# Kernel tuning notes

Hardware: AMD Instinct MI355X
Metric: run time of the kernel (lower is better)

## Reference

```python
import jax, jax.numpy as jnp
import numpy as np

B = 4
NB = 8192   # points per batch
MB = 2048   # query points per batch
C_IN = 64
RADII = (0.2, 0.4)
NSAMPLES = (16, 32)
EPS = 1e-5


def setup_inputs() -> dict:
    key = jax.random.key(0)
    ks = jax.random.split(key, 8)
    inp = {}
    inp["xyz"] = jax.random.uniform(ks[0], (B * NB, 3), jnp.float32)
    inp["features"] = jax.random.normal(ks[1], (B * NB, C_IN), jnp.float32)
    inp["new_xyz"] = jax.random.uniform(ks[2], (B * MB, 3), jnp.float32)
    inp["xyz_batch_cnt"] = jnp.full((B,), NB, jnp.int32)
    inp["new_xyz_batch_cnt"] = jnp.full((B,), MB, jnp.int32)
    cin = C_IN + 3  # use_xyz=True concatenates relative xyz
    for s in range(2):
        k0, k1 = jax.random.split(ks[3 + s])
        inp[f"w{s}0"] = jax.random.normal(k0, (128, cin), jnp.float32) * (2.0 / cin) ** 0.5
        inp[f"g{s}0"] = jnp.ones((128,), jnp.float32)
        inp[f"b{s}0"] = jnp.zeros((128,), jnp.float32)
        inp[f"w{s}1"] = jax.random.normal(k1, (128, 128), jnp.float32) * (2.0 / 128) ** 0.5
        inp[f"g{s}1"] = jnp.ones((128,), jnp.float32)
        inp[f"b{s}1"] = jnp.zeros((128,), jnp.float32)
    return inp


def _ball_query(new_b, xyz_b, radius, nsample):
    # new_b: (B, M, 3), xyz_b: (B, N, 3)
    n = xyz_b.shape[1]
    # squared distances via the quadratic expansion (avoids (B,M,N,3) temp)
    d2 = (jnp.sum(new_b * new_b, -1)[:, :, None]
          + jnp.sum(xyz_b * xyz_b, -1)[:, None, :]
          - 2.0 * jnp.einsum('bmc,bnc->bmn', new_b, xyz_b))
    in_ball = d2 < radius * radius
    # first-nsample-in-original-order semantics of the CUDA ball query
    order_key = jnp.where(in_ball, jnp.arange(n, dtype=jnp.int32)[None, None, :], n)
    idxs = jnp.sort(order_key, axis=-1)[..., :nsample]        # (B, M, nsample)
    valid = idxs < n
    first = idxs[..., :1]                                     # pad with first found idx
    idx = jnp.where(valid, idxs, first)
    empty = ~valid[..., 0]                                    # no neighbor in ball
    idx = jnp.where(empty[..., None], 0, idx)
    return idx, empty


def _bn_relu(x, g, b):
    # training-mode BatchNorm2d over (M, nsample) per channel, then ReLU
    mean = jnp.mean(x, axis=(0, 1))
    var = jnp.var(x, axis=(0, 1))
    return jax.nn.relu((x - mean) * jax.lax.rsqrt(var + EPS) * g + b)


def _scale(xyz_b, feat_b, new_b, radius, nsample, w0, g0, b0, w1, g1, b1):
    idx, empty = _ball_query(new_b, xyz_b, radius, nsample)
    gather = jax.vmap(lambda pts, i: pts[i])                  # per-batch gather
    gx = gather(xyz_b, idx) - new_b[:, :, None, :]            # (B, M, ns, 3)
    gf = gather(feat_b, idx)                                  # (B, M, ns, C)
    g = jnp.concatenate([gx, gf], axis=-1)                    # use_xyz=True
    g = jnp.where(empty[..., None, None], 0.0, g)             # zero empty balls
    g = g.reshape(-1, nsample, g.shape[-1])                   # (M_total, ns, 3+C)
    h = _bn_relu(jnp.einsum('mnc,oc->mno', g, w0), g0, b0)    # shared 1x1 conv
    h = _bn_relu(jnp.einsum('mnc,oc->mno', h, w1), g1, b1)
    return jnp.max(h, axis=1)                                 # max_pool over ns


def reference(xyz, features, new_xyz, xyz_batch_cnt, new_xyz_batch_cnt,
              w00, g00, b00, w01, g01, b01,
              w10, g10, b10, w11, g11, b11):
    b = xyz_batch_cnt.shape[0]
    xyz_b = xyz.reshape(b, -1, 3)
    feat_b = features.reshape(b, -1, features.shape[-1])
    new_b = new_xyz.reshape(b, -1, 3)
    f0 = _scale(xyz_b, feat_b, new_b, RADII[0], NSAMPLES[0], w00, g00, b00, w01, g01, b01)
    f1 = _scale(xyz_b, feat_b, new_b, RADII[1], NSAMPLES[1], w10, g10, b10, w11, g11, b11)
    return new_xyz, jnp.concatenate([f0, f1], axis=1)         # (M_total, 256)
```

## Files before the change

### kernel.cpp

```cpp
#include <hip/hip_runtime.h>
#include <stdio.h>

#define NBP   8192
#define MTOT  8192
#define CIN   64
#define CO    128

#define EPR(...) do { fprintf(stderr, __VA_ARGS__); fflush(stderr); } while (0)

typedef short short8 __attribute__((ext_vector_type(8)));
typedef float floatx4 __attribute__((ext_vector_type(4)));
typedef unsigned short ushort;
typedef ushort ushort4v __attribute__((ext_vector_type(4)));

__device__ __forceinline__ ushort f2b(float f)
{
    union { unsigned int i; float f; } x; x.f = f;
    return (ushort)((x.i + 0x7fffu + ((x.i >> 16) & 1u)) >> 16);
}
__device__ __forceinline__ float b2f(ushort u)
{
    union { unsigned int i; float f; } x; x.i = ((unsigned int)u) << 16;
    return x.f;
}
__device__ __forceinline__ void split_rne(float v, ushort& h, ushort& l)
{
    ushort hh = f2b(v);
    h = hh; l = f2b(v - b2f(hh));
}

__global__ void __launch_bounds__(256, 1) StackSAModuleMSG_85761906966880_kernel(
    const float* __restrict__ xyz, const float* __restrict__ nxyz,
    float* __restrict__ out, float* __restrict__ stats,
    const float* __restrict__ feat, ushort* __restrict__ fh,
    int* __restrict__ idx0, int* __restrict__ idx1,
    int* __restrict__ empty0, int* __restrict__ empty1,
    const float* __restrict__ w00, const float* __restrict__ w01,
    const float* __restrict__ w10, const float* __restrict__ w11,
    ushort* __restrict__ wh00, ushort* __restrict__ wl00,
    ushort* __restrict__ wh01, ushort* __restrict__ wl01,
    ushort* __restrict__ wh10, ushort* __restrict__ wl10,
    ushort* __restrict__ wh11, ushort* __restrict__ wl11)
{
    if (blockIdx.x < MTOT/4) {
        const double r2a = 0.2 * 0.2;
        const double r2b = 0.4 * 0.4;
        int m    = blockIdx.x * 4 + (threadIdx.x >> 6);
        int lane = threadIdx.x & 63;
        int b    = m >> 11;
        int base = b * NBP;

        double nx = (double)nxyz[3*m+0];
        double ny = (double)nxyz[3*m+1];
        double nz = (double)nxyz[3*m+2];
        double nn = nx*nx + ny*ny + nz*nz;

        int cnt0 = 0, cnt1 = 0;
        int first0 = base, first1 = base;
        unsigned long long lt = (1ull << lane) - 1ull;

        for (int j = 0; j < NBP; j += 64) {
            int gi = base + j + lane;
            double px = (double)xyz[3*gi+0];
            double py = (double)xyz[3*gi+1];
            double pz = (double)xyz[3*gi+2];
            double pp = px*px + py*py + pz*pz;
            double dt = nx*px + ny*py + nz*pz;
            double d2 = nn + pp - 2.0*dt;
            bool in0 = d2 < r2a;
            bool in1 = d2 < r2b;
            unsigned long long m0 = __ballot(in0);
            unsigned long long m1 = __ballot(in1);
            if (in0) {
                int p0 = cnt0 + __popcll(m0 & lt);
                if (p0 < 16) idx0[m*16 + p0] = gi;
            }
            if (in1) {
                int p1 = cnt1 + __popcll(m1 & lt);
                if (p1 < 32) idx1[m*32 + p1] = gi;
            }
            if (cnt0 == 0 && m0) first0 = base + j + (__ffsll((long long)m0) - 1);
            if (cnt1 == 0 && m1) first1 = base + j + (__ffsll((long long)m1) - 1);
            cnt0 += __popcll(m0);
            cnt1 += __popcll(m1);
            if (cnt0 >= 16 && cnt1 >= 32) break;
        }
        int c0 = cnt0 < 16 ? cnt0 : 16;
        int c1 = cnt1 < 32 ? cnt1 : 32;
        if (lane >= c0 && lane < 16) idx0[m*16 + lane] = first0;
        if (lane >= c1 && lane < 32) idx1[m*32 + lane] = first1;
        if (lane == 0) { empty0[m] = (cnt0 == 0); empty1[m] = (cnt1 == 0); }
    } else {
        int i = (blockIdx.x - MTOT/4) * 256 + threadIdx.x;
        if (i < 1024) stats[i] = 0.f;
        if (i < MTOT*3) out[i] = nxyz[i];
        if (i < 128*128) {
            split_rne(w01[i], wh01[i], wl01[i]);
            split_rne(w11[i], wh11[i], wl11[i]);
        }
        if (i < 128*96) {
            int o = i / 96, kd = i - o*96;
            int c = (kd < 64) ? (kd + 3) : ((kd < 67) ? (kd - 64) : -1);
            float a = (c >= 0) ? w00[o*67 + c] : 0.f;
            split_rne(a, wh00[i], wl00[i]);
            float b = (c >= 0) ? w10[o*67 + c] : 0.f;
            split_rne(b, wh10[i], wl10[i]);
        }
        {
            float4 v = *(const float4*)(feat + (size_t)4*i);
            ushort4v h;
            h[0] = f2b(v.x); h[1] = f2b(v.y); h[2] = f2b(v.z); h[3] = f2b(v.w);
            *(ushort4v*)(fh + (size_t)4*i) = h;
        }
    }
}

template<int NS, int GM>
__device__ __forceinline__ void gather128(
    const ushort* __restrict__ fh,
    const float* __restrict__ xyz, const float* __restrict__ nxyz,
    const int* __restrict__ idx, unsigned em, int m0, int t, ushort* ah)
{
    constexpr int ROWS = NS*GM;
    const long long ib = (long long)m0 * NS;
    const short8 Z8 = {0,0,0,0,0,0,0,0};
#pragma unroll
    for (int e = t; e < ROWS*8; e += 256) {
        int n = e >> 3, c8 = e & 7;
        int gi = idx[ib + n];
        short8 v = *(const short8*)(fh + (size_t)gi*CIN + 8*c8);
        if ((em >> (n / NS)) & 1u) v = Z8;
        *(short8*)(ah + n*136 + 8*c8) = v;
    }
#pragma unroll
    for (int e = t; e < ROWS*4; e += 256) {
        int n = e >> 2, k3 = e & 3;
        short8 v = Z8;
        if (k3 == 0) {
            int g = n / NS;
            if (!((em >> g) & 1u)) {
                int gi = idx[ib + n];
#pragma unroll
                for (int c = 0; c < 3; c++)
                    v[c] = (short)f2b(xyz[3*gi+c] - nxyz[3*(m0+g)+c]);
            }
        }
        *(short8*)(ah + n*136 + 64 + 8*k3) = v;
    }
}

template<int NS, int GM>
__device__ __forceinline__ void stats1_body(
    const ushort* __restrict__ fh,
    const float* __restrict__ xyz, const float* __restrict__ nxyz,
    const int* __restrict__ idx, const int* __restrict__ empty,
    const ushort* __restrict__ wh0, float* __restrict__ part,
    int bx, int t, ushort* ah)
{
    int m0 = bx * GM;
    int wv = t >> 6, lane = t & 63, l16 = lane & 15, qo = lane >> 4;
    int n0 = 32*wv;

    short8 bh[3][2];
#pragma unroll
    for (int ks = 0; ks < 3; ks++)
#pragma unroll
        for (int nt = 0; nt < 2; nt++)
            bh[ks][nt] = *(const short8*)(wh0 +
                (long long)(n0 + 16*nt + l16)*96 + ks*32 + qo*8);

    unsigned em = 0;
#pragma unroll
    for (int g = 0; g < GM; g++) em |= (empty[m0 + g] ? 1u : 0u) << g;
    gather128<NS, GM>(fh, xyz, nxyz, idx, em, m0, t, ah);
    __syncthreads();

    floatx4 acc[8][2];
#pragma unroll
    for (int i = 0; i < 8; i++) {
        acc[i][0] = (floatx4){0.f,0.f,0.f,0.f};
        acc[i][1] = (floatx4){0.f,0.f,0.f,0.f};
    }
#pragma unroll
    for (int ks = 0; ks < 3; ks++) {
        int kb = ks*32 + qo*8;
#pragma unroll
        for (int mt = 0; mt < 8; mt++) {
            int ao = (16*mt + l16)*136 + kb;
            short8 fh8 = *(const short8*)(ah + ao);
#pragma unroll
            for (int nt = 0; nt < 2; nt++)
                acc[mt][nt] = __builtin_amdgcn_mfma_f32_16x16x32_bf16(
                                  fh8, bh[ks][nt], acc[mt][nt], 0, 0, 0);
        }
    }

    float sum[2] = {0.f,0.f}, sq[2] = {0.f,0.f};
#pragma unroll
    for (int mt = 0; mt < 8; mt++)
#pragma unroll
        for (int nt = 0; nt < 2; nt++)
#pragma unroll
            for (int r = 0; r < 4; r++) {
                float a = acc[mt][nt][r];
                sum[nt] += a; sq[nt] = fmaf(a, a, sq[nt]);
            }
#pragma unroll
    for (int nt = 0; nt < 2; nt++) {
        sum[nt] += __shfl_xor(sum[nt], 16); sum[nt] += __shfl_xor(sum[nt], 32);
        sq[nt]  += __shfl_xor(sq[nt],  16); sq[nt]  += __shfl_xor(sq[nt],  32);
    }
    if (lane < 16) {
#pragma unroll
        for (int nt = 0; nt < 2; nt++) {
            int c = n0 + 16*nt + lane;
            part[(long long)bx*256 + c]       = sum[nt];
            part[(long long)bx*256 + 128 + c] = sq[nt];
        }
    }
}

__global__ void __launch_bounds__(256, 4) sa_stats1_both(
    const ushort* __restrict__ fh,
    const float* __restrict__ xyz, const float* __restrict__ nxyz,
    const int* __restrict__ idx0, const int* __restrict__ empty0,
    const ushort* __restrict__ wh00, float* __restrict__ partA,
    const int* __restrict__ idx1, const int* __restrict__ empty1,
    const ushort* __restrict__ wh10, float* __restrict__ partB)
{
    __shared__ ushort ah[128*136];
    int t = threadIdx.x;
    if (blockIdx.x < MTOT/8)
        stats1_body<16,8>(fh, xyz, nxyz, idx0, empty0, wh00, partA,
                          blockIdx.x, t, ah);
    else
        stats1_body<32,4>(fh, xyz, nxyz, idx1, empty1, wh10, partB,
                          blockIdx.x - MTOT/8, t, ah);
}

template<int NS, int GM>
__device__ __forceinline__ void fused_body(
    const ushort* __restrict__ fh,
    const float* __restrict__ xyz, const float* __restrict__ nxyz,
    const int* __restrict__ idx, const int* __restrict__ empty,
    const ushort* __restrict__ wh0, const ushort* __restrict__ wl0,
    const ushort* __restrict__ wh1, const ushort* __restrict__ wl1,
    const float* __restrict__ g0, const float* __restrict__ b0,
    const float* __restrict__ s1sum, const float* __restrict__ s1sq,
    float* __restrict__ part, float* __restrict__ mxo, float* __restrict__ mno,
    float invN, int bx, int t,
    ushort* ah, float* kv, float* sv)
{
    const int TPG = NS/16;
    int m0 = bx * GM;
    int wv = t >> 6, lane = t & 63, l16 = lane & 15, qo = lane >> 4;
    int n0 = 32*wv;

    if (t < 128) {
        float mean = s1sum[t] * invN;
        float var  = s1sq[t] * invN - mean * mean;
        float k    = rsqrtf(var + 1e-5f) * g0[t];
        kv[t] = k;
        sv[t] = b0[t] - mean * k;
    }

    const long long wrow0 = (long long)(n0 + l16);
    const long long wrow1 = (long long)(n0 + 16 + l16);

    short8 wsh[2][2], wsl[2][2];
#pragma unroll
    for (int ks = 0; ks < 2; ks++) {
        wsh[ks][0] = *(const short8*)(wh0 + wrow0*96 + ks*32 + qo*8);
        wsl[ks][0] = *(const short8*)(wl0 + wrow0*96 + ks*32 + qo*8);
        wsh[ks][1] = *(const short8*)(wh0 + wrow1*96 + ks*32 + qo*8);
        wsl[ks][1] = *(const short8*)(wl0 + wrow1*96 + ks*32 + qo*8);
    }

    unsigned em = 0;
#pragma unroll
    for (int g = 0; g < GM; g++) em |= (empty[m0 + g] ? 1u : 0u) << g;
    gather128<NS, GM>(fh, xyz, nxyz, idx, em, m0, t, ah);
    __syncthreads();

    floatx4 acc[8][2];
#pragma unroll
    for (int i = 0; i < 8; i++) {
        acc[i][0] = (floatx4){0.f,0.f,0.f,0.f};
        acc[i][1] = (floatx4){0.f,0.f,0.f,0.f};
    }

#pragma unroll
    for (int mt = 0; mt < 8; mt++) {
        short8 fh8 = *(const short8*)(ah + (16*mt + l16)*136 + qo*8);
#pragma unroll
        for (int nt = 0; nt < 2; nt++) {
            acc[mt][nt] = __builtin_amdgcn_mfma_f32_16x16x32_bf16(
                              fh8, wsl[0][nt], acc[mt][nt], 0, 0, 0);
            acc[mt][nt] = __builtin_amdgcn_mfma_f32_16x16x32_bf16(
                              fh8, wsh[0][nt], acc[mt][nt], 0, 0, 0);
        }
    }
    wsh[0][0] = *(const short8*)(wh0 + wrow0*96 + 64 + qo*8);
    wsl[0][0] = *(const short8*)(wl0 + wrow0*96 + 64 + qo*8);
    wsh[0][1] = *(const short8*)(wh0 + wrow1*96 + 64 + qo*8);
    wsl[0][1] = *(const short8*)(wl0 + wrow1*96 + 64 + qo*8);
#pragma unroll
    for (int mt = 0; mt < 8; mt++) {
        short8 fh8 = *(const short8*)(ah + (16*mt + l16)*136 + 32 + qo*8);
#pragma unroll
        for (int nt = 0; nt < 2; nt++) {
            acc[mt][nt] = __builtin_amdgcn_mfma_f32_16x16x32_bf16(
                              fh8, wsl[1][nt], acc[mt][nt], 0, 0, 0);
            acc[mt][nt] = __builtin_amdgcn_mfma_f32_16x16x32_bf16(
                              fh8, wsh[1][nt], acc[mt][nt], 0, 0, 0);
        }
    }
#pragma unroll
    for (int mt = 0; mt < 8; mt++) {
        short8 fh8 = *(const short8*)(ah + (16*mt + l16)*136 + 64 + qo*8);
#pragma unroll
        for (int nt = 0; nt < 2; nt++) {
            acc[mt][nt] = __builtin_amdgcn_mfma_f32_16x16x32_bf16(
                              fh8, wsl[0][nt], acc[mt][nt], 0, 0, 0);
            acc[mt][nt] = __builtin_amdgcn_mfma_f32_16x16x32_bf16(
                              fh8, wsh[0][nt], acc[mt][nt], 0, 0, 0);
        }
    }

    __syncthreads();

#pragma unroll
    for (int nt = 0; nt < 2; nt++) {
        int c = n0 + 16*nt + l16;
        float k = kv[c], s = sv[c];
#pragma unroll
        for (int mt = 0; mt < 8; mt++) {
            int rbase = 16*mt + qo*4;
#pragma unroll
            for (int r = 0; r < 4; r += 2) {
                float h0 = fmaxf(fmaf(acc[mt][nt][r],   k, s), 0.f);
                float h1 = fmaxf(fmaf(acc[mt][nt][r+1], k, s), 0.f);
                unsigned int pk;
                asm("v_cvt_pk_bf16_f32 %0, %1, %2"
                    : "=v"(pk) : "v"(h0), "v"(h1));
                ah[(rbase + r    )*136 + c] = (ushort)(pk & 0xffffu);
                ah[(rbase + r + 1)*136 + c] = (ushort)(pk >> 16);
            }
        }
    }

#pragma unroll
    for (int ks = 0; ks < 2; ks++) {
        wsh[ks][0] = *(const short8*)(wh1 + wrow0*128 + ks*32 + qo*8);
        wsl[ks][0] = *(const short8*)(wl1 + wrow0*128 + ks*32 + qo*8);
        wsh[ks][1] = *(const short8*)(wh1 + wrow1*128 + ks*32 + qo*8);
        wsl[ks][1] = *(const short8*)(wl1 + wrow1*128 + ks*32 + qo*8);
    }
    __syncthreads();

#pragma unroll
    for (int i = 0; i < 8; i++) {
        acc[i][0] = (floatx4){0.f,0.f,0.f,0.f};
        acc[i][1] = (floatx4){0.f,0.f,0.f,0.f};
    }
#pragma unroll
    for (int mt = 0; mt < 8; mt++) {
        short8 fh8 = *(const short8*)(ah + (16*mt + l16)*136 + qo*8);
#pragma unroll
        for (int nt = 0; nt < 2; nt++) {
            acc[mt][nt] = __builtin_amdgcn_mfma_f32_16x16x32_bf16(
                              fh8, wsl[0][nt], acc[mt][nt], 0, 0, 0);
            acc[mt][nt] = __builtin_amdgcn_mfma_f32_16x16x32_bf16(
                              fh8, wsh[0][nt], acc[mt][nt], 0, 0, 0);
        }
    }
    wsh[0][0] = *(const short8*)(wh1 + wrow0*128 + 64 + qo*8);
    wsl[0][0] = *(const short8*)(wl1 + wrow0*128 + 64 + qo*8);
    wsh[0][1] = *(const short8*)(wh1 + wrow1*128 + 64 + qo*8);
    wsl[0][1] = *(const short8*)(wl1 + wrow1*128 + 64 + qo*8);
#pragma unroll
    for (int mt = 0; mt < 8; mt++) {
        short8 fh8 = *(const short8*)(ah + (16*mt + l16)*136 + 32 + qo*8);
#pragma unroll
        for (int nt = 0; nt < 2; nt++) {
            acc[mt][nt] = __builtin_amdgcn_mfma_f32_16x16x32_bf16(
                              fh8, wsl[1][nt], acc[mt][nt], 0, 0, 0);
            acc[mt][nt] = __builtin_amdgcn_mfma_f32_16x16x32_bf16(
                              fh8, wsh[1][nt], acc[mt][nt], 0, 0, 0);
        }
    }
    wsh[1][0] = *(const short8*)(wh1 + wrow0*128 + 96 + qo*8);
    wsl[1][0] = *(const short8*)(wl1 + wrow0*128 + 96 + qo*8);
    wsh[1][1] = *(const short8*)(wh1 + wrow1*128 + 96 + qo*8);
    wsl[1][1] = *(const short8*)(wl1 + wrow1*128 + 96 + qo*8);
#pragma unroll
    for (int mt = 0; mt < 8; mt++) {
        short8 fh8 = *(const short8*)(ah + (16*mt + l16)*136 + 64 + qo*8);
#pragma unroll
        for (int nt = 0; nt < 2; nt++) {
            acc[mt][nt] = __builtin_amdgcn_mfma_f32_16x16x32_bf16(
                              fh8, wsl[0][nt], acc[mt][nt], 0, 0, 0);
            acc[mt][nt] = __builtin_amdgcn_mfma_f32_16x16x32_bf16(
                              fh8, wsh[0][nt], acc[mt][nt], 0, 0, 0);
        }
    }
#pragma unroll
    for (int mt = 0; mt < 8; mt++) {
        short8 fh8 = *(const short8*)(ah + (16*mt + l16)*136 + 96 + qo*8);
#pragma unroll
        for (int nt = 0; nt < 2; nt++) {
            acc[mt][nt] = __builtin_amdgcn_mfma_f32_16x16x32_bf16(
                              fh8, wsl[1][nt], acc[mt][nt], 0, 0, 0);
            acc[mt][nt] = __builtin_amdgcn_mfma_f32_16x16x32_bf16(
                              fh8, wsh[1][nt], acc[mt][nt], 0, 0, 0);
        }
    }

    float sum[2] = {0.f,0.f}, sq[2] = {0.f,0.f};
    float Mx[GM][2], Mn[GM][2];
#pragma unroll
    for (int g = 0; g < GM; g++) {
        Mx[g][0] = -3.4e38f; Mx[g][1] = -3.4e38f;
        Mn[g][0] =  3.4e38f; Mn[g][1] =  3.4e38f;
    }
#pragma unroll
    for (int mt = 0; mt < 8; mt++) {
        int gg = mt / TPG;
#pragma unroll
        for (int nt = 0; nt < 2; nt++)
#pragma unroll
            for (int r = 0; r < 4; r++) {
                float a = acc[mt][nt][r];
                sum[nt] += a; sq[nt] = fmaf(a, a, sq[nt]);
                Mx[gg][nt] = fmaxf(Mx[gg][nt], a);
                Mn[gg][nt] = fminf(Mn[gg][nt], a);
            }
    }
#pragma unroll
    for (int nt = 0; nt < 2; nt++) {
        sum[nt] += __shfl_xor(sum[nt], 16); sum[nt] += __shfl_xor(sum[nt], 32);
        sq[nt]  += __shfl_xor(sq[nt],  16); sq[nt]  += __shfl_xor(sq[nt],  32);
#pragma unroll
        for (int g = 0; g < GM; g++) {
            Mx[g][nt] = fmaxf(Mx[g][nt], __shfl_xor(Mx[g][nt], 16));
            Mx[g][nt] = fmaxf(Mx[g][nt], __shfl_xor(Mx[g][nt], 32));
            Mn[g][nt] = fminf(Mn[g][nt], __shfl_xor(Mn[g][nt], 16));
            Mn[g][nt] = fminf(Mn[g][nt], __shfl_xor(Mn[g][nt], 32));
        }
    }
    if (lane < 16) {
#pragma unroll
        for (int nt = 0; nt < 2; nt++) {
            int c = n0 + 16*nt + lane;
            part[(long long)bx*256 + c]       = sum[nt];
            part[(long long)bx*256 + 128 + c] = sq[nt];
#pragma unroll
            for (int g = 0; g < GM; g++) {
                mxo[(long long)(m0+g)*128 + c] = Mx[g][nt];
                mno[(long long)(m0+g)*128 + c] = Mn[g][nt];
            }
        }
    }
}

__global__ void __launch_bounds__(256, 4) sa_fused_both(
    const ushort* __restrict__ fh,
    const float* __restrict__ xyz, const float* __restrict__ nxyz,
    const int* __restrict__ idx0, const int* __restrict__ empty0,
    const ushort* __restrict__ wh00, const ushort* __restrict__ wl00,
    const ushort* __restrict__ wh01, const ushort* __restrict__ wl01,
    const float* __restrict__ g00, const float* __restrict__ b00,
    const float* __restrict__ s1sumA, const float* __restrict__ s1sqA,
    float* __restrict__ partA, float* __restrict__ mx0, float* __restrict__ mn0,
    float invN0,
    const int* __restrict__ idx1, const int* __restrict__ empty1,
    const ushort* __restrict__ wh10, const ushort* __restrict__ wl10,
    const ushort* __restrict__ wh11, const ushort* __restrict__ wl11,
    const float* __restrict__ g10, const float* __restrict__ b10,
    const float* __restrict__ s1sumB, const float* __restrict__ s1sqB,
    float* __restrict__ partB, float* __restrict__ mx1, float* __restrict__ mn1,
    float invN1)
{
    __shared__ ushort ah[128*136];
    __shared__ float kv[128], sv[128];
    int t = threadIdx.x;
    if (blockIdx.x < MTOT/8)
        fused_body<16,8>(fh, xyz, nxyz, idx0, empty0,
                         wh00, wl00, wh01, wl01, g00, b00, s1sumA, s1sqA,
                         partA, mx0, mn0, invN0, blockIdx.x, t,
                         ah, kv, sv);
    else
        fused_body<32,4>(fh, xyz, nxyz, idx1, empty1,
                         wh10, wl10, wh11, wl11, g10, b10, s1sumB, s1sqB,
                         partB, mx1, mn1, invN1, blockIdx.x - MTOT/8, t,
                         ah, kv, sv);
}

__global__ void __launch_bounds__(256, 1) sa_reduce2(
    const float* __restrict__ partA, int nbA, float* __restrict__ dstA,
    const float* __restrict__ partB, int nbB, float* __restrict__ dstB)
{
    __shared__ float red[256];
    int t = threadIdx.x;
    const float* part; float* dst; int nb, b;
    if (blockIdx.x < 256) { part = partA; dst = dstA; nb = nbA; b = blockIdx.x; }
    else                  { part = partB; dst = dstB; nb = nbB; b = blockIdx.x - 256; }
    float s = 0.f;
    for (int i = t; i < nb; i += 256) s += part[(long long)i*256 + b];
    red[t] = s;
    __syncthreads();
    for (int off = 128; off > 0; off >>= 1) {
        if (t < off) red[t] += red[t + off];
        __syncthreads();
    }
    if (t == 0) dst[b] = red[0];
}

__global__ void __launch_bounds__(256, 1) sa_pass3b(
    const float* __restrict__ mx0, const float* __restrict__ mn0,
    const float* __restrict__ g01, const float* __restrict__ b01,
    const float* __restrict__ mx1, const float* __restrict__ mn1,
    const float* __restrict__ g11, const float* __restrict__ b11,
    const float* __restrict__ stats, float* __restrict__ outp,
    float invN0, float invN1)
{
    int i = blockIdx.x * 256 + threadIdx.x;
    int m = i >> 8, o = i & 255;
    bool sc1 = o >= 128;
    int oc = o & 127;
    const float* sm = sc1 ? (stats + 768) : (stats + 256);
    const float* sp = sc1 ? (stats + 896) : (stats + 384);
    float invN = sc1 ? invN1 : invN0;
    float gg   = sc1 ? g11[oc] : g01[oc];
    float bb   = sc1 ? b11[oc] : b01[oc];
    float mean = sm[oc] * invN;
    float var  = sp[oc] * invN - mean * mean;
    float k    = rsqrtf(var + 1e-5f) * gg;
    float sh   = bb - mean * k;
    long long mi = (long long)m * 128 + oc;
    float v;
    if (k >= 0.f) v = sc1 ? mx1[mi] : mx0[mi];
    else          v = sc1 ? mn1[mi] : mn0[mi];
    float r = fmaf(v, k, sh);
    outp[i] = r > 0.f ? r : 0.f;
}

extern "C" void kernel_launch(void* const* d_in, const int* in_sizes, int n_in,
                              void* d_out, int out_size, void* d_ws, size_t ws_size,
                              hipStream_t stream)
{
    const float* xyz  = (const float*)d_in[0];
    const float* feat = (const float*)d_in[1];
    const float* nxyz = (const float*)d_in[2];
    const float* w00 = (const float*)d_in[5];
    const float* g00 = (const float*)d_in[6];
    const float* b00 = (const float*)d_in[7];
    const float* w01 = (const float*)d_in[8];
    const float* g01 = (const float*)d_in[9];
    const float* b01 = (const float*)d_in[10];
    const float* w10 = (const float*)d_in[11];
    const float* g10 = (const float*)d_in[12];
    const float* b10 = (const float*)d_in[13];
    const float* w11 = (const float*)d_in[14];
    const float* g11 = (const float*)d_in[15];
    const float* b11 = (const float*)d_in[16];
    float* out = (float*)d_out;

    char*  wsb    = (char*)d_ws;
    float* stats  = (float*)(wsb);
    int*   idx0   = (int*)(wsb + 4096);
    int*   idx1   = (int*)(wsb + 4096 + 524288);
    int*   empty0 = (int*)(wsb + 4096 + 524288 + 1048576);
    int*   empty1 = (int*)(wsb + 4096 + 524288 + 1048576 + 32768);
    ushort* fh    = (ushort*)(wsb + 2000000);
    float* mx0    = (float*)(wsb + 150000000);
    float* mn0    = (float*)(wsb + 155000000);
    float* mx1    = (float*)(wsb + 160000000);
    float* mn1    = (float*)(wsb + 165000000);
    ushort* wh01  = (ushort*)(wsb + 170000000);
    ushort* wl01  = (ushort*)(wsb + 171000000);
    ushort* wh11  = (ushort*)(wsb + 172000000);
    ushort* wl11  = (ushort*)(wsb + 173000000);
    ushort* wh00  = (ushort*)(wsb + 174000000);
    ushort* wl00  = (ushort*)(wsb + 175000000);
    ushort* wh10  = (ushort*)(wsb + 176000000);
    ushort* wl10  = (ushort*)(wsb + 177000000);
    float* partA  = (float*)(wsb + 180000000);
    float* partB  = (float*)(wsb + 183000000);

    const float invN0 = 1.0f / (float)(MTOT*16);
    const float invN1 = 1.0f / (float)(MTOT*32);
    float* fout = out + MTOT*3;

    StackSAModuleMSG_85761906966880_kernel<<<MTOT/4 + 2048, 256, 0, stream>>>(
        xyz, nxyz, out, stats, feat, fh,
        idx0, idx1, empty0, empty1,
        w00, w01, w10, w11,
        wh00, wl00, wh01, wl01, wh10, wl10, wh11, wl11);

    sa_stats1_both<<<MTOT/8 + MTOT/4, 256, 0, stream>>>(
        fh, xyz, nxyz,
        idx0, empty0, wh00, partA,
        idx1, empty1, wh10, partB);

    sa_reduce2<<<512, 256, 0, stream>>>(partA, MTOT/8, stats + 0,
                                        partB, MTOT/4, stats + 512);

    sa_fused_both<<<MTOT/8 + MTOT/4, 256, 0, stream>>>(
        fh, xyz, nxyz,
        idx0, empty0, wh00, wl00, wh01, wl01, g00, b00,
        stats + 0, stats + 128, partA, mx0, mn0, invN0,
        idx1, empty1, wh10, wl10, wh11, wl11, g10, b10,
        stats + 512, stats + 640, partB, mx1, mn1, invN1);

    sa_reduce2<<<512, 256, 0, stream>>>(partA, MTOT/8, stats + 256,
                                        partB, MTOT/4, stats + 768);

    sa_pass3b<<<(MTOT*256)/256, 256, 0, stream>>>(
        mx0, mn0, g01, b01, mx1, mn1, g11, b11, stats, fout, invN0, invN1);

    hipError_t e = hipGetLastError();
    if (e != hipSuccess) EPR("[KL] enqueue err=%d (%s)\n", (int)e, hipGetErrorString(e));
}
```

Measured before the change: 208.8 us.

## Replace per-block BN partials and reduce kernels with striped atomic accumulation

Result: faster. 201.0 us (-3.7%).

```diff
diff --git a/kernel.cpp b/kernel.cpp
--- a/kernel.cpp
+++ b/kernel.cpp
@@ -31,7 +31,7 @@
 
 __global__ void __launch_bounds__(256, 1) StackSAModuleMSG_85761906966880_kernel(
     const float* __restrict__ xyz, const float* __restrict__ nxyz,
-    float* __restrict__ out, float* __restrict__ stats,
+    float* __restrict__ out, float* __restrict__ scop,
     const float* __restrict__ feat, ushort* __restrict__ fh,
     int* __restrict__ idx0, int* __restrict__ idx1,
     int* __restrict__ empty0, int* __restrict__ empty1,
@@ -92,7 +92,7 @@
         if (lane == 0) { empty0[m] = (cnt0 == 0); empty1[m] = (cnt1 == 0); }
     } else {
         int i = (blockIdx.x - MTOT/4) * 256 + threadIdx.x;
-        if (i < 1024) stats[i] = 0.f;
+        if (i < 16384) scop[i] = 0.f;
         if (i < MTOT*3) out[i] = nxyz[i];
         if (i < 128*128) {
             split_rne(w01[i], wh01[i], wl01[i]);
@@ -154,7 +154,7 @@
     const ushort* __restrict__ fh,
     const float* __restrict__ xyz, const float* __restrict__ nxyz,
     const int* __restrict__ idx, const int* __restrict__ empty,
-    const ushort* __restrict__ wh0, float* __restrict__ part,
+    const ushort* __restrict__ wh0, float* __restrict__ sdst,
     int bx, int t, ushort* ah)
 {
     int m0 = bx * GM;
@@ -211,11 +211,12 @@
         sq[nt]  += __shfl_xor(sq[nt],  16); sq[nt]  += __shfl_xor(sq[nt],  32);
     }
     if (lane < 16) {
+        float* dst = sdst + (bx & 15) * 256;
 #pragma unroll
         for (int nt = 0; nt < 2; nt++) {
             int c = n0 + 16*nt + lane;
-            part[(long long)bx*256 + c]       = sum[nt];
-            part[(long long)bx*256 + 128 + c] = sq[nt];
+            atomicAdd(&dst[c],       sum[nt]);
+            atomicAdd(&dst[128 + c], sq[nt]);
         }
     }
 }
@@ -224,18 +225,18 @@
     const ushort* __restrict__ fh,
     const float* __restrict__ xyz, const float* __restrict__ nxyz,
     const int* __restrict__ idx0, const int* __restrict__ empty0,
-    const ushort* __restrict__ wh00, float* __restrict__ partA,
+    const ushort* __restrict__ wh00,
     const int* __restrict__ idx1, const int* __restrict__ empty1,
-    const ushort* __restrict__ wh10, float* __restrict__ partB)
+    const ushort* __restrict__ wh10, float* __restrict__ scop)
 {
     __shared__ ushort ah[128*136];
     int t = threadIdx.x;
     if (blockIdx.x < MTOT/8)
-        stats1_body<16,8>(fh, xyz, nxyz, idx0, empty0, wh00, partA,
-                          blockIdx.x, t, ah);
+        stats1_body<16,8>(fh, xyz, nxyz, idx0, empty0, wh00,
+                          scop + 0, blockIdx.x, t, ah);
     else
-        stats1_body<32,4>(fh, xyz, nxyz, idx1, empty1, wh10, partB,
-                          blockIdx.x - MTOT/8, t, ah);
+        stats1_body<32,4>(fh, xyz, nxyz, idx1, empty1, wh10,
+                          scop + 4096, blockIdx.x - MTOT/8, t, ah);
 }
 
 template<int NS, int GM>
@@ -246,8 +247,8 @@
     const ushort* __restrict__ wh0, const ushort* __restrict__ wl0,
     const ushort* __restrict__ wh1, const ushort* __restrict__ wl1,
     const float* __restrict__ g0, const float* __restrict__ b0,
-    const float* __restrict__ s1sum, const float* __restrict__ s1sq,
-    float* __restrict__ part, float* __restrict__ mxo, float* __restrict__ mno,
+    const float* __restrict__ s1cop, float* __restrict__ s2dst,
+    float* __restrict__ mxo, float* __restrict__ mno,
     float invN, int bx, int t,
     ushort* ah, float* kv, float* sv)
 {
@@ -257,8 +258,14 @@
     int n0 = 32*wv;
 
     if (t < 128) {
-        float mean = s1sum[t] * invN;
-        float var  = s1sq[t] * invN - mean * mean;
+        float sm = 0.f, sqv = 0.f;
+#pragma unroll
+        for (int cp = 0; cp < 16; cp++) {
+            sm  += s1cop[cp*256 + t];
+            sqv += s1cop[cp*256 + 128 + t];
+        }
+        float mean = sm * invN;
+        float var  = sqv * invN - mean * mean;
         float k    = rsqrtf(var + 1e-5f) * g0[t];
         kv[t] = k;
         sv[t] = b0[t] - mean * k;
@@ -449,11 +456,12 @@
         }
     }
     if (lane < 16) {
+        float* dst = s2dst + (bx & 15) * 256;
 #pragma unroll
         for (int nt = 0; nt < 2; nt++) {
             int c = n0 + 16*nt + lane;
-            part[(long long)bx*256 + c]       = sum[nt];
-            part[(long long)bx*256 + 128 + c] = sq[nt];
+            atomicAdd(&dst[c],       sum[nt]);
+            atomicAdd(&dst[128 + c], sq[nt]);
 #pragma unroll
             for (int g = 0; g < GM; g++) {
                 mxo[(long long)(m0+g)*128 + c] = Mx[g][nt];
@@ -470,50 +478,27 @@
     const ushort* __restrict__ wh00, const ushort* __restrict__ wl00,
     const ushort* __restrict__ wh01, const ushort* __restrict__ wl01,
     const float* __restrict__ g00, const float* __restrict__ b00,
-    const float* __restrict__ s1sumA, const float* __restrict__ s1sqA,
-    float* __restrict__ partA, float* __restrict__ mx0, float* __restrict__ mn0,
-    float invN0,
+    float* __restrict__ mx0, float* __restrict__ mn0, float invN0,
     const int* __restrict__ idx1, const int* __restrict__ empty1,
     const ushort* __restrict__ wh10, const ushort* __restrict__ wl10,
     const ushort* __restrict__ wh11, const ushort* __restrict__ wl11,
     const float* __restrict__ g10, const float* __restrict__ b10,
-    const float* __restrict__ s1sumB, const float* __restrict__ s1sqB,
-    float* __restrict__ partB, float* __restrict__ mx1, float* __restrict__ mn1,
-    float invN1)
+    float* __restrict__ mx1, float* __restrict__ mn1, float invN1,
+    float* __restrict__ scop)
 {
     __shared__ ushort ah[128*136];
     __shared__ float kv[128], sv[128];
     int t = threadIdx.x;
     if (blockIdx.x < MTOT/8)
         fused_body<16,8>(fh, xyz, nxyz, idx0, empty0,
-                         wh00, wl00, wh01, wl01, g00, b00, s1sumA, s1sqA,
-                         partA, mx0, mn0, invN0, blockIdx.x, t,
-                         ah, kv, sv);
+                         wh00, wl00, wh01, wl01, g00, b00,
+                         scop + 0, scop + 8192,
+                         mx0, mn0, invN0, blockIdx.x, t, ah, kv, sv);
     else
         fused_body<32,4>(fh, xyz, nxyz, idx1, empty1,
-                         wh10, wl10, wh11, wl11, g10, b10, s1sumB, s1sqB,
-                         partB, mx1, mn1, invN1, blockIdx.x - MTOT/8, t,
-                         ah, kv, sv);
-}
-
-__global__ void __launch_bounds__(256, 1) sa_reduce2(
-    const float* __restrict__ partA, int nbA, float* __restrict__ dstA,
-    const float* __restrict__ partB, int nbB, float* __restrict__ dstB)
-{
-    __shared__ float red[256];
-    int t = threadIdx.x;
-    const float* part; float* dst; int nb, b;
-    if (blockIdx.x < 256) { part = partA; dst = dstA; nb = nbA; b = blockIdx.x; }
-    else                  { part = partB; dst = dstB; nb = nbB; b = blockIdx.x - 256; }
-    float s = 0.f;
-    for (int i = t; i < nb; i += 256) s += part[(long long)i*256 + b];
-    red[t] = s;
-    __syncthreads();
-    for (int off = 128; off > 0; off >>= 1) {
-        if (t < off) red[t] += red[t + off];
-        __syncthreads();
-    }
-    if (t == 0) dst[b] = red[0];
+                         wh10, wl10, wh11, wl11, g10, b10,
+                         scop + 4096, scop + 12288,
+                         mx1, mn1, invN1, blockIdx.x - MTOT/8, t, ah, kv, sv);
 }
 
 __global__ void __launch_bounds__(256, 1) sa_pass3b(
@@ -521,20 +506,25 @@
     const float* __restrict__ g01, const float* __restrict__ b01,
     const float* __restrict__ mx1, const float* __restrict__ mn1,
     const float* __restrict__ g11, const float* __restrict__ b11,
-    const float* __restrict__ stats, float* __restrict__ outp,
+    const float* __restrict__ scop, float* __restrict__ outp,
     float invN0, float invN1)
 {
     int i = blockIdx.x * 256 + threadIdx.x;
     int m = i >> 8, o = i & 255;
     bool sc1 = o >= 128;
     int oc = o & 127;
-    const float* sm = sc1 ? (stats + 768) : (stats + 256);
-    const float* sp = sc1 ? (stats + 896) : (stats + 384);
+    const float* sc = sc1 ? (scop + 12288) : (scop + 8192);
     float invN = sc1 ? invN1 : invN0;
     float gg   = sc1 ? g11[oc] : g01[oc];
     float bb   = sc1 ? b11[oc] : b01[oc];
-    float mean = sm[oc] * invN;
-    float var  = sp[oc] * invN - mean * mean;
+    float sm = 0.f, sp = 0.f;
+#pragma unroll
+    for (int cp = 0; cp < 16; cp++) {
+        sm += sc[cp*256 + oc];
+        sp += sc[cp*256 + 128 + oc];
+    }
+    float mean = sm * invN;
+    float var  = sp * invN - mean * mean;
     float k    = rsqrtf(var + 1e-5f) * gg;
     float sh   = bb - mean * k;
     long long mi = (long long)m * 128 + oc;
@@ -567,7 +557,6 @@
     float* out = (float*)d_out;
 
     char*  wsb    = (char*)d_ws;
-    float* stats  = (float*)(wsb);
     int*   idx0   = (int*)(wsb + 4096);
     int*   idx1   = (int*)(wsb + 4096 + 524288);
     int*   empty0 = (int*)(wsb + 4096 + 524288 + 1048576);
@@ -585,39 +574,32 @@
     ushort* wl00  = (ushort*)(wsb + 175000000);
     ushort* wh10  = (ushort*)(wsb + 176000000);
     ushort* wl10  = (ushort*)(wsb + 177000000);
-    float* partA  = (float*)(wsb + 180000000);
-    float* partB  = (float*)(wsb + 183000000);
+    float* scop   = (float*)(wsb + 180000000);
 
     const float invN0 = 1.0f / (float)(MTOT*16);
     const float invN1 = 1.0f / (float)(MTOT*32);
     float* fout = out + MTOT*3;
 
     StackSAModuleMSG_85761906966880_kernel<<<MTOT/4 + 2048, 256, 0, stream>>>(
-        xyz, nxyz, out, stats, feat, fh,
+        xyz, nxyz, out, scop, feat, fh,
         idx0, idx1, empty0, empty1,
         w00, w01, w10, w11,
         wh00, wl00, wh01, wl01, wh10, wl10, wh11, wl11);
 
     sa_stats1_both<<<MTOT/8 + MTOT/4, 256, 0, stream>>>(
         fh, xyz, nxyz,
-        idx0, empty0, wh00, partA,
-        idx1, empty1, wh10, partB);
-
-    sa_reduce2<<<512, 256, 0, stream>>>(partA, MTOT/8, stats + 0,
-                                        partB, MTOT/4, stats + 512);
+        idx0, empty0, wh00,
+        idx1, empty1, wh10, scop);
 
     sa_fused_both<<<MTOT/8 + MTOT/4, 256, 0, stream>>>(
         fh, xyz, nxyz,
         idx0, empty0, wh00, wl00, wh01, wl01, g00, b00,
-        stats + 0, stats + 128, partA, mx0, mn0, invN0,
+        mx0, mn0, invN0,
         idx1, empty1, wh10, wl10, wh11, wl11, g10, b10,
-        stats + 512, stats + 640, partB, mx1, mn1, invN1);
-
-    sa_reduce2<<<512, 256, 0, stream>>>(partA, MTOT/8, stats + 256,
-                                        partB, MTOT/4, stats + 768);
+        mx1, mn1, invN1, scop);
 
     sa_pass3b<<<(MTOT*256)/256, 256, 0, stream>>>(
-        mx0, mn0, g01, b01, mx1, mn1, g11, b11, stats, fout, invN0, invN1);
+        mx0, mn0, g01, b01, mx1, mn1, g11, b11, scop, fout, invN0, invN1);
 
     hipError_t e = hipGetLastError();
     if (e != hipSuccess) EPR("[KL] enqueue err=%d (%s)\n", (int)e, hipGetErrorString(e));
```
